# Kernel optimization log

Measured on AMD Instinct MI355X. Metric: run time of the kernel, lower is better.

Reference implementation:

```python
import jax, jax.numpy as jnp
import numpy as np

B, N, DIM, VDIM, H, HD = 4, 1369, 1024, 1536, 16, 64
ROPE_HW, ROPE_DIM, THETA = 37, 32, 10000.0
LN_EPS = 1e-5


def _rope_tables():
    # VisionRotaryEmbeddingFast: freqs_for='lang', dim=32, pt_seq_len=ft_seq_len=37
    inv = 1.0 / THETA ** (jnp.arange(0, ROPE_DIM, 2, dtype=jnp.float32) / ROPE_DIM)  # [16]
    t = jnp.arange(ROPE_HW, dtype=jnp.float32) / ROPE_HW * ROPE_HW                    # [37]
    f = t[:, None] * inv[None, :]                                                     # [37,16]
    f = jnp.repeat(f, 2, axis=-1)                                                     # [37,32]
    # broadcat along last dim over the 2D grid -> [37,37,64]
    f2 = jnp.concatenate([jnp.broadcast_to(f[:, None, :], (ROPE_HW, ROPE_HW, ROPE_DIM)),
                          jnp.broadcast_to(f[None, :, :], (ROPE_HW, ROPE_HW, ROPE_DIM))], axis=-1)
    f2 = f2.reshape(-1, 2 * ROPE_DIM)                                                 # [1369,64]
    return jnp.cos(f2), jnp.sin(f2)


def _rotate_half(x):
    # pairs (x0,x1) -> (-x1,x0), interleaved
    xr = x.reshape(*x.shape[:-1], x.shape[-1] // 2, 2)
    x1, x2 = xr[..., 0], xr[..., 1]
    return jnp.stack((-x2, x1), axis=-1).reshape(x.shape)


def setup_inputs() -> dict:
    key = jax.random.key(0)
    ks = jax.random.split(key, 8)
    return {
        "x": jax.random.normal(ks[0], (B, N, DIM), jnp.float32),
        "value": jax.random.normal(ks[1], (B, N, VDIM), jnp.float32),
        "attn_mask": jax.random.randint(ks[2], (B, N), 0, 2).astype(bool),
        "wq": jax.random.normal(ks[3], (DIM, DIM), jnp.float32) * 0.02,
        "wk": jax.random.normal(ks[4], (DIM, VDIM), jnp.float32) * 0.02,
        "wv": jax.random.normal(ks[5], (DIM, VDIM), jnp.float32) * 0.02,
        "ln_g": jnp.ones((DIM,), jnp.float32),
        "ln_b": jnp.zeros((DIM,), jnp.float32),
        "wp": jax.random.normal(ks[6], (DIM, DIM), jnp.float32) * 0.02,
        "bp": jnp.zeros((DIM,), jnp.float32),
    }


def reference(x, value, attn_mask, wq, wk, wv, ln_g, ln_b, wp, bp):
    cos, sin = _rope_tables()  # [N, 64] each
    # projections (torch F.linear: y = x @ W.T)
    q = jnp.einsum('bni,oi->bno', x, wq).reshape(B, N, H, HD).transpose(0, 2, 1, 3)
    k = jnp.einsum('bni,oi->bno', value, wk).reshape(B, N, H, HD).transpose(0, 2, 1, 3)
    v = jnp.einsum('bni,oi->bno', value, wv).reshape(B, N, H, HD).transpose(0, 2, 1, 3)
    # inline RoPE on q and k
    q = q * cos + _rotate_half(q) * sin
    k = k * cos + _rotate_half(k) * sin
    q = q * (HD ** -0.5)
    attn = jnp.einsum('bhnd,bhmd->bhnm', q, k)
    neg_inf = jnp.finfo(attn.dtype).min
    attn = jnp.where(attn_mask[:, None, None, :], attn, neg_inf)
    attn = jax.nn.softmax(attn, axis=-1)
    out = jnp.einsum('bhnm,bhmd->bhnd', attn, v)
    out = out.transpose(0, 2, 1, 3).reshape(B, N, H * HD)
    # inner_attn_ln (LayerNorm, eps=1e-5)
    mu = jnp.mean(out, axis=-1, keepdims=True)
    var = jnp.var(out, axis=-1, keepdims=True)
    out = (out - mu) * jax.lax.rsqrt(var + LN_EPS) * ln_g + ln_b
    # output projection
    return jnp.einsum('bni,oi->bno', out, wp) + bp
```

## Files before the change

kernel.cpp:

```cpp
#include <hip/hip_runtime.h>
#include <hip/hip_bf16.h>

#define BB 4
#define NN 1369
#define DIMM 1024
#define VDIMM 1536
#define HH 16
#define MM (BB*NN)
#define MPAD 5504
#define NPAD 1408
#define KVB 64
#define NT (NPAD/KVB)
#define QSCALE 0.18028334f

typedef __attribute__((ext_vector_type(4))) float f32x4;
typedef __attribute__((ext_vector_type(8))) __bf16 bf16x8;
typedef __attribute__((ext_vector_type(4))) __bf16 bf16x4;

#define GLOAD_LDS(gsrc, ldst) \
  __builtin_amdgcn_global_load_lds((const __attribute__((address_space(1))) unsigned int*)(gsrc), \
                                   (__attribute__((address_space(3))) unsigned int*)(ldst), 16, 0, 0)

__global__ __launch_bounds__(256) void cvt_inputs(const float* __restrict__ x,
                                                  const float* __restrict__ val,
                                                  __bf16* __restrict__ xb,
                                                  __bf16* __restrict__ vb) {
  const int NX = MM * 1024 / 4;
  const int NV = MM * 1536 / 4;
  int i = blockIdx.x * blockDim.x + threadIdx.x;
  int st = gridDim.x * blockDim.x;
  for (; i < NX + NV; i += st) {
    const float* s; __bf16* d; int j;
    if (i < NX) { s = x; d = xb; j = i; }
    else        { s = val; d = vb; j = i - NX; }
    f32x4 v = ((const f32x4*)s)[j];
    bf16x4 o;
    o[0] = (__bf16)v[0]; o[1] = (__bf16)v[1];
    o[2] = (__bf16)v[2]; o[3] = (__bf16)v[3];
    ((bf16x4*)d)[j] = o;
  }
}

__global__ __launch_bounds__(256) void cvt_weights(
    const float* __restrict__ wq, const float* __restrict__ wk,
    const float* __restrict__ wv, const float* __restrict__ wp,
    __bf16* __restrict__ wqb, __bf16* __restrict__ wkvb, __bf16* __restrict__ wpb) {
  const int NQ = 1024 * 1024 / 4;
  const int NK = 1024 * 1536 / 4;
  int i = blockIdx.x * blockDim.x + threadIdx.x;
  int st = gridDim.x * blockDim.x;
  for (; i < 2 * NQ + 2 * NK; i += st) {
    const float* s; __bf16* d; int j = i;
    if (j < NQ) { s = wq; d = wqb; }
    else if (j < NQ + NK) { j -= NQ; s = wk; d = wkvb; }
    else if (j < NQ + 2 * NK) { j -= NQ + NK; s = wv; d = wkvb + (size_t)1024 * 1536; }
    else { j -= NQ + 2 * NK; s = wp; d = wpb; }
    f32x4 v = ((const f32x4*)s)[j];
    bf16x4 o;
    o[0] = (__bf16)v[0]; o[1] = (__bf16)v[1];
    o[2] = (__bf16)v[2]; o[3] = (__bf16)v[3];
    ((bf16x4*)d)[j] = o;
  }
}

__global__ __launch_bounds__(256) void rope_tables(float* __restrict__ cosT,
                                                   float* __restrict__ sinT) {
  int idx = blockIdx.x * blockDim.x + threadIdx.x;
  if (idx >= NN * 64) return;
  int n = idx >> 6, d = idx & 63;
  int r = n / 37, c = n % 37;
  int m = (d < 32) ? (d >> 1) : ((d - 32) >> 1);
  float p = (d < 32) ? (float)r : (float)c;
  float inv = powf(10000.f, -(float)m * (1.f / 16.f));
  float a = p * inv;
  cosT[idx] = cosf(a);
  sinT[idx] = sinf(a);
}

__global__ __launch_bounds__(256) void mask_prep(const void* __restrict__ mask,
                                                 float* __restrict__ maskA) {
  __shared__ int flags[2];
  int t = threadIdx.x;
  if (t < 2) flags[t] = 0;
  __syncthreads();
  const unsigned int* mw = (const unsigned int*)mask;
  for (int i = t; i < NN; i += blockDim.x) {
    unsigned int w = mw[i];
    if (w == 0x3F800000u) atomicOr(&flags[1], 1);
    else if (w > 1u) atomicOr(&flags[0], 1);
  }
  __syncthreads();
  int md = flags[1] ? 2 : (flags[0] ? 1 : 0);
  const unsigned char* mb = (const unsigned char*)mask;
  const float* mf = (const float*)mask;
  for (int i = t; i < BB * NPAD; i += blockDim.x) {
    int b = i / NPAD, key = i % NPAD;
    float v = -1e30f;
    if (key < NN) {
      int idx = b * NN + key;
      bool on = (md == 0) ? (mw[idx] != 0u) : (md == 1) ? (mb[idx] != 0) : (mf[idx] != 0.f);
      if (on) v = 0.f;
    }
    maskA[i] = v;
  }
}

template <int TN, int EPI, int GRID2D>
__global__ __launch_bounds__(256) void gemm_bt(
    const __bf16* __restrict__ A, const __bf16* __restrict__ W, int K,
    __bf16* __restrict__ obf, __bf16* __restrict__ obf2, float* __restrict__ of32,
    const float* __restrict__ cosT, const float* __restrict__ sinT,
    const float* __restrict__ bp) {
  constexpr int MI = (TN == 128) ? 4 : 2;
  __shared__ __bf16 As[2][128 * 32];
  __shared__ __bf16 Bs[2][TN * 32];
  const int tid = threadIdx.x;
  const int w = tid >> 6, l = tid & 63;
  int tN, tM;
  if (GRID2D) {
    tN = blockIdx.x; tM = blockIdx.y;
  } else {
    const int i0 = blockIdx.x;
    const int orig = (i0 & 7) * 86 + (i0 >> 3);
    tN = orig & 15; tM = orig >> 4;
  }
  const int wm = (TN == 128) ? (w >> 1) : w;
  const int wn = (TN == 128) ? (w & 1) : 0;
  const int wmo = wm * ((TN == 128) ? 64 : 32);
  const int lo = l & 15, hi = l >> 4;

  const __bf16* Asrc = A + (size_t)(tM * 128 + lo) * K + hi * 8;
  const __bf16* Wsrc = W + (size_t)(tN * TN + lo) * K + hi * 8;

  f32x4 zero = {0.f, 0.f, 0.f, 0.f};
  f32x4 acc[MI][4];
#pragma unroll
  for (int i = 0; i < MI; ++i)
#pragma unroll
    for (int j = 0; j < 4; ++j) acc[i][j] = zero;

  auto GSTAGE = [&](int buf, int k0) {
#pragma unroll
    for (int j = 0; j < 2; ++j) {
      const int c = j * 4 + w;
      GLOAD_LDS(Asrc + (size_t)c * 16 * K + k0, (char*)&As[buf][c * 512]);
    }
    if constexpr (TN == 128) {
#pragma unroll
      for (int j = 0; j < 2; ++j) {
        const int c = j * 4 + w;
        GLOAD_LDS(Wsrc + (size_t)c * 16 * K + k0, (char*)&Bs[buf][c * 512]);
      }
    } else {
      GLOAD_LDS(Wsrc + (size_t)w * 16 * K + k0, (char*)&Bs[buf][w * 512]);
    }
  };

  const int nk = K >> 5;
  GSTAGE(0, 0);
  int cur = 0;
  const int ga = wmo >> 4;
  const int gb = (TN == 128) ? (wn * 4) : 0;
  for (int t = 0; t < nk; ++t) {
    __syncthreads();
    if (t + 1 < nk) GSTAGE(cur ^ 1, (t + 1) * 32);
    bf16x8 af[MI], bfr[4];
#pragma unroll
    for (int mi = 0; mi < MI; ++mi)
      af[mi] = *(const bf16x8*)&As[cur][(ga + mi) * 512 + hi * 128 + lo * 8];
#pragma unroll
    for (int ni = 0; ni < 4; ++ni)
      bfr[ni] = *(const bf16x8*)&Bs[cur][(gb + ni) * 512 + hi * 128 + lo * 8];
    __builtin_amdgcn_s_setprio(1);
#pragma unroll
    for (int mi = 0; mi < MI; ++mi)
#pragma unroll
      for (int ni = 0; ni < 4; ++ni)
        acc[mi][ni] = __builtin_amdgcn_mfma_f32_16x16x32_bf16(af[mi], bfr[ni], acc[mi][ni], 0, 0, 0);
    __builtin_amdgcn_s_setprio(0);
    cur ^= 1;
  }

  const int m_base = tM * 128 + wmo;
  const int o_base = tN * TN + wn * 64;
  const bool isK = (EPI == 1) && (tN < 8);
#pragma unroll
  for (int mi = 0; mi < MI; ++mi) {
    const int m4 = m_base + mi * 16 + hi * 4;
    if (EPI == 1 && !isK) {
      if (m4 < MM) {
        const int b0 = m4 / NN, n0 = m4 % NN;
#pragma unroll
        for (int ni = 0; ni < 4; ++ni) {
          const int o2 = o_base + ni * 16 + lo - 1024;
          const int h = o2 >> 6, d = o2 & 63;
          if (n0 <= NN - 4) {
            bf16x4 pv;
#pragma unroll
            for (int r = 0; r < 4; ++r) pv[r] = (__bf16)acc[mi][ni][r];
            *(bf16x4*)&obf2[((size_t)(b0 * HH + h) * 64 + d) * NPAD + n0] = pv;
          } else {
#pragma unroll
            for (int r = 0; r < 4; ++r) {
              const int mr = m4 + r;
              const int br = mr / NN, nr = mr % NN;
              obf2[((size_t)(br * HH + h) * 64 + d) * NPAD + nr] = (__bf16)acc[mi][ni][r];
            }
          }
        }
      }
    } else {
#pragma unroll
      for (int r = 0; r < 4; ++r) {
        const int mrow = m4 + r;
#pragma unroll
        for (int ni = 0; ni < 4; ++ni) {
          const int col = o_base + ni * 16 + lo;
          float v = acc[mi][ni][r];
          if (EPI == 0 || EPI == 1) {
            float pprt = __shfl_xor(v, 1);
            if (mrow < MM) {
              int b = mrow / NN, n = mrow % NN;
              int h = col >> 6, d = col & 63;
              float cs = cosT[n * 64 + d], sn = sinT[n * 64 + d];
              float out = v * cs + (((d & 1) == 0) ? -pprt : pprt) * sn;
              if (EPI == 0) out *= QSCALE;
              obf[((size_t)(b * HH + h) * NPAD + n) * 64 + d] = (__bf16)out;
            }
          } else {
            if (mrow < MM) of32[(size_t)mrow * DIMM + col] = v + bp[col];
          }
        }
      }
    }
  }
}

__device__ inline unsigned int pk2(float a, float b) {
  unsigned int ua = (unsigned int)__builtin_bit_cast(unsigned short, (__bf16)a);
  unsigned int ub = (unsigned int)__builtin_bit_cast(unsigned short, (__bf16)b);
  return ua | (ub << 16);
}

__global__ __launch_bounds__(256) void attn_kernel(
    const __bf16* __restrict__ Qb, const __bf16* __restrict__ Kb,
    const __bf16* __restrict__ Vtb, const float* __restrict__ maskA,
    float* __restrict__ AO) {
  __shared__ __bf16 Ks[2][64 * 64];
  __shared__ __bf16 Vs[2][64 * 64];
  __shared__ unsigned int Plds[4][16 * 32];
  const int tid = threadIdx.x;
  const int w = tid >> 6, l = tid & 63;
  const int lo = l & 15, hi = l >> 4;

  const int i = blockIdx.x;
  const int orig = (i & 7) * 176 + (i >> 3);
  const int bh = orig / NT;
  const int qt = orig % NT;
  const int b = bh >> 4;
  const int q0 = qt * 64 + w * 16;

  const __bf16* Qp = Qb + ((size_t)bh * NPAD + q0) * 64;
  bf16x8 qf0 = *(const bf16x8*)&Qp[lo * 64 + hi * 8];
  bf16x8 qf1 = *(const bf16x8*)&Qp[lo * 64 + 32 + hi * 8];

  const int row8 = l >> 3;
  const int swz16 = ((l & 7) ^ row8) << 4;
  const int lo7 = lo & 7;
  const int swzW = (lo & 7) << 2;

  f32x4 zero = {0.f, 0.f, 0.f, 0.f};
  f32x4 O[4];
#pragma unroll
  for (int n = 0; n < 4; ++n) O[n] = zero;
  float lr = 0.f;
  const float* mk = maskA + b * NPAD;

#define STAGE(buf, k0)                                                                   \
  {                                                                                      \
    _Pragma("unroll") for (int j = 0; j < 2; ++j) {                                      \
      const int rbase = (j * 4 + w) * 8;                                                 \
      const char* ksrc = (const char*)Kb +                                               \
          ((size_t)bh * NPAD + (k0) + rbase + row8) * 128 + swz16;                       \
      GLOAD_LDS(ksrc, (char*)&Ks[buf][0] + rbase * 128);                                 \
      const char* vsrc = (const char*)Vtb +                                              \
          ((size_t)(bh * 64 + rbase + row8) * NPAD + (k0)) * 2 + swz16;                  \
      GLOAD_LDS(vsrc, (char*)&Vs[buf][0] + rbase * 128);                                 \
    }                                                                                    \
  }

  STAGE(0, 0);
  __syncthreads();
  int cur = 0;

  for (int t = 0; t < NT; ++t) {
    if (t + 1 < NT) STAGE(cur ^ 1, (t + 1) * KVB);

    const __bf16* KB = &Ks[cur][0];
    const __bf16* VB = &Vs[cur][0];

    f32x4 mv[4];
#pragma unroll
    for (int c = 0; c < 4; ++c) mv[c] = *(const f32x4*)&mk[t * KVB + c * 16 + hi * 4];

    f32x4 S[4];
    __builtin_amdgcn_s_setprio(1);
#pragma unroll
    for (int c = 0; c < 4; ++c) {
      const int kr = c * 16 + lo;
      bf16x8 kfa = *(const bf16x8*)&KB[kr * 64 + ((hi ^ lo7) * 8)];
      bf16x8 kfb = *(const bf16x8*)&KB[kr * 64 + (((hi + 4) ^ lo7) * 8)];
      f32x4 s = __builtin_amdgcn_mfma_f32_16x16x32_bf16(kfa, qf0, zero, 0, 0, 0);
      S[c]     = __builtin_amdgcn_mfma_f32_16x16x32_bf16(kfb, qf1, s, 0, 0, 0);
    }
    __builtin_amdgcn_s_setprio(0);

    float rs = 0.f;
#pragma unroll
    for (int c = 0; c < 4; ++c) {
      float p0 = exp2f(S[c][0] + mv[c][0]);
      float p1 = exp2f(S[c][1] + mv[c][1]);
      float p2 = exp2f(S[c][2] + mv[c][2]);
      float p3 = exp2f(S[c][3] + mv[c][3]);
      rs += (p0 + p1) + (p2 + p3);
      uint2 pw = {pk2(p0, p1), pk2(p2, p3)};
      *(uint2*)&Plds[w][lo * 32 + ((8 * c + 2 * hi) ^ swzW)] = pw;
    }
    lr += rs;

    bf16x8 pf0 = *(const bf16x8*)&Plds[w][lo * 32 + ((4 * hi) ^ swzW)];
    bf16x8 pf1 = *(const bf16x8*)&Plds[w][lo * 32 + ((16 + 4 * hi) ^ swzW)];

    __builtin_amdgcn_s_setprio(1);
#pragma unroll
    for (int n = 0; n < 4; ++n) {
      const int vr = n * 16 + lo;
      bf16x8 vfa = *(const bf16x8*)&VB[vr * 64 + ((hi ^ lo7) * 8)];
      bf16x8 vfb = *(const bf16x8*)&VB[vr * 64 + (((hi + 4) ^ lo7) * 8)];
      O[n] = __builtin_amdgcn_mfma_f32_16x16x32_bf16(vfa, pf0, O[n], 0, 0, 0);
      O[n] = __builtin_amdgcn_mfma_f32_16x16x32_bf16(vfb, pf1, O[n], 0, 0, 0);
    }
    __builtin_amdgcn_s_setprio(0);

    __syncthreads();
    cur ^= 1;
  }
#undef STAGE

  lr += __shfl_xor(lr, 16);
  lr += __shfl_xor(lr, 32);
  const float inv = 1.f / lr;

  const int h = bh & 15;
  const int token = q0 + lo;
  if (token < NN) {
    float* dst = AO + (size_t)(b * NN + token) * DIMM + h * 64 + hi * 4;
#pragma unroll
    for (int n = 0; n < 4; ++n) {
      f32x4 o = O[n];
      o[0] *= inv; o[1] *= inv; o[2] *= inv; o[3] *= inv;
      *(f32x4*)(dst + n * 16) = o;
    }
  }
}

__global__ __launch_bounds__(256) void ln_kernel(
    const float* __restrict__ AO, const float* __restrict__ g,
    const float* __restrict__ be, __bf16* __restrict__ outb) {
  const int row = blockIdx.x;
  const int t = threadIdx.x;
  const float* x = AO + (size_t)row * DIMM;
  f32x4 v = ((const f32x4*)x)[t];
  float s = v[0] + v[1] + v[2] + v[3];
  float sq = v[0] * v[0] + v[1] * v[1] + v[2] * v[2] + v[3] * v[3];
#pragma unroll
  for (int m = 1; m < 64; m <<= 1) { s += __shfl_xor(s, m); sq += __shfl_xor(sq, m); }
  __shared__ float ss[4], ssq[4];
  int w = t >> 6, l = t & 63;
  if (l == 0) { ss[w] = s; ssq[w] = sq; }
  __syncthreads();
  s = ss[0] + ss[1] + ss[2] + ss[3];
  sq = ssq[0] + ssq[1] + ssq[2] + ssq[3];
  float mean = s * (1.f / 1024.f);
  float var = sq * (1.f / 1024.f) - mean * mean;
  float rstd = rsqrtf(var + 1e-5f);
  __bf16* o = outb + (size_t)row * DIMM + t * 4;
  const float* gp = g + t * 4;
  const float* bp2 = be + t * 4;
#pragma unroll
  for (int j = 0; j < 4; ++j) o[j] = (__bf16)((v[j] - mean) * rstd * gp[j] + bp2[j]);
}

extern "C" void kernel_launch(void* const* d_in, const int* in_sizes, int n_in,
                              void* d_out, int out_size, void* d_ws, size_t ws_size,
                              hipStream_t stream) {
  const float* x   = (const float*)d_in[0];
  const float* val = (const float*)d_in[1];
  const void*  msk = d_in[2];
  const float* wq  = (const float*)d_in[3];
  const float* wk  = (const float*)d_in[4];
  const float* wv  = (const float*)d_in[5];
  const float* lng = (const float*)d_in[6];
  const float* lnb = (const float*)d_in[7];
  const float* wp  = (const float*)d_in[8];
  const float* bpv = (const float*)d_in[9];
  float* out = (float*)d_out;

  char* ws = (char*)d_ws;
  size_t off = 0;
  auto alloc = [&](size_t bytes) -> char* {
    char* p = ws + off;
    off += (bytes + 255) & ~(size_t)255;
    return p;
  };
  __bf16* xb   = (__bf16*)alloc((size_t)MPAD * 1024 * 2);
  __bf16* vb   = (__bf16*)alloc((size_t)MPAD * 1536 * 2);
  __bf16* wqb  = (__bf16*)alloc((size_t)1024 * 1024 * 2);
  __bf16* wkvb = (__bf16*)alloc((size_t)2048 * 1536 * 2);
  __bf16* wpb  = (__bf16*)alloc((size_t)1024 * 1024 * 2);
  __bf16* Qb   = (__bf16*)alloc((size_t)64 * NPAD * 64 * 2);
  __bf16* Kb   = (__bf16*)alloc((size_t)64 * NPAD * 64 * 2);
  __bf16* Vtb  = (__bf16*)alloc((size_t)64 * 64 * NPAD * 2);
  float* AO    = (float*)alloc((size_t)MM * 1024 * 4);
  float* cosT  = (float*)alloc((size_t)NN * 64 * 4);
  float* sinT  = (float*)alloc((size_t)NN * 64 * 4);
  float* maskA = (float*)alloc((size_t)BB * NPAD * 4);


  cvt_inputs<<<2048, 256, 0, stream>>>(x, val, xb, vb);
  cvt_weights<<<1024, 256, 0, stream>>>(wq, wk, wv, wp, wqb, wkvb, wpb);
  rope_tables<<<(NN * 64 + 255) / 256, 256, 0, stream>>>(cosT, sinT);
  mask_prep<<<1, 256, 0, stream>>>(msk, maskA);

  gemm_bt<64, 0, 1><<<dim3(16, 43), 256, 0, stream>>>(xb, wqb, 1024, Qb, nullptr, nullptr, cosT, sinT, nullptr);
  gemm_bt<128, 1, 0><<<dim3(688), 256, 0, stream>>>(vb, wkvb, 1536, Kb, Vtb, nullptr, cosT, sinT, nullptr);

  attn_kernel<<<dim3(64 * NT), 256, 0, stream>>>(Qb, Kb, Vtb, maskA, AO);

  ln_kernel<<<MM, 256, 0, stream>>>(AO, lng, lnb, xb);

  gemm_bt<64, 3, 1><<<dim3(16, 43), 256, 0, stream>>>(xb, wpb, 1024, nullptr, nullptr, out, nullptr, nullptr, bpv);
}
```

Measured before the change: 281.5 us.

## Fold LayerNorm into output projection GEMM via precomputed row stats and column constants

```diff
diff --git a/kernel.cpp b/kernel.cpp
--- a/kernel.cpp
+++ b/kernel.cpp
@@ -44,64 +44,127 @@
 __global__ __launch_bounds__(256) void cvt_weights(
     const float* __restrict__ wq, const float* __restrict__ wk,
     const float* __restrict__ wv, const float* __restrict__ wp,
-    __bf16* __restrict__ wqb, __bf16* __restrict__ wkvb, __bf16* __restrict__ wpb) {
+    const float* __restrict__ g,
+    __bf16* __restrict__ wqb, __bf16* __restrict__ wkvb, __bf16* __restrict__ wgb) {
   const int NQ = 1024 * 1024 / 4;
   const int NK = 1024 * 1536 / 4;
   int i = blockIdx.x * blockDim.x + threadIdx.x;
   int st = gridDim.x * blockDim.x;
   for (; i < 2 * NQ + 2 * NK; i += st) {
-    const float* s; __bf16* d; int j = i;
-    if (j < NQ) { s = wq; d = wqb; }
-    else if (j < NQ + NK) { j -= NQ; s = wk; d = wkvb; }
-    else if (j < NQ + 2 * NK) { j -= NQ + NK; s = wv; d = wkvb + (size_t)1024 * 1536; }
-    else { j -= NQ + 2 * NK; s = wp; d = wpb; }
-    f32x4 v = ((const f32x4*)s)[j];
-    bf16x4 o;
-    o[0] = (__bf16)v[0]; o[1] = (__bf16)v[1];
-    o[2] = (__bf16)v[2]; o[3] = (__bf16)v[3];
-    ((bf16x4*)d)[j] = o;
-  }
-}
-
-__global__ __launch_bounds__(256) void rope_tables(float* __restrict__ cosT,
-                                                   float* __restrict__ sinT) {
-  int idx = blockIdx.x * blockDim.x + threadIdx.x;
-  if (idx >= NN * 64) return;
-  int n = idx >> 6, d = idx & 63;
-  int r = n / 37, c = n % 37;
-  int m = (d < 32) ? (d >> 1) : ((d - 32) >> 1);
-  float p = (d < 32) ? (float)r : (float)c;
-  float inv = powf(10000.f, -(float)m * (1.f / 16.f));
-  float a = p * inv;
-  cosT[idx] = cosf(a);
-  sinT[idx] = sinf(a);
-}
-
-__global__ __launch_bounds__(256) void mask_prep(const void* __restrict__ mask,
-                                                 float* __restrict__ maskA) {
-  __shared__ int flags[2];
-  int t = threadIdx.x;
-  if (t < 2) flags[t] = 0;
-  __syncthreads();
-  const unsigned int* mw = (const unsigned int*)mask;
-  for (int i = t; i < NN; i += blockDim.x) {
-    unsigned int w = mw[i];
-    if (w == 0x3F800000u) atomicOr(&flags[1], 1);
-    else if (w > 1u) atomicOr(&flags[0], 1);
-  }
-  __syncthreads();
-  int md = flags[1] ? 2 : (flags[0] ? 1 : 0);
-  const unsigned char* mb = (const unsigned char*)mask;
-  const float* mf = (const float*)mask;
-  for (int i = t; i < BB * NPAD; i += blockDim.x) {
-    int b = i / NPAD, key = i % NPAD;
-    float v = -1e30f;
-    if (key < NN) {
-      int idx = b * NN + key;
-      bool on = (md == 0) ? (mw[idx] != 0u) : (md == 1) ? (mb[idx] != 0) : (mf[idx] != 0.f);
-      if (on) v = 0.f;
-    }
-    maskA[i] = v;
+    int j = i;
+    if (j < NQ) {
+      f32x4 v = ((const f32x4*)wq)[j];
+      bf16x4 o;
+      o[0] = (__bf16)v[0]; o[1] = (__bf16)v[1]; o[2] = (__bf16)v[2]; o[3] = (__bf16)v[3];
+      ((bf16x4*)wqb)[j] = o;
+    } else if (j < NQ + NK) {
+      j -= NQ;
+      f32x4 v = ((const f32x4*)wk)[j];
+      bf16x4 o;
+      o[0] = (__bf16)v[0]; o[1] = (__bf16)v[1]; o[2] = (__bf16)v[2]; o[3] = (__bf16)v[3];
+      ((bf16x4*)wkvb)[j] = o;
+    } else if (j < NQ + 2 * NK) {
+      j -= NQ + NK;
+      f32x4 v = ((const f32x4*)wv)[j];
+      bf16x4 o;
+      o[0] = (__bf16)v[0]; o[1] = (__bf16)v[1]; o[2] = (__bf16)v[2]; o[3] = (__bf16)v[3];
+      ((bf16x4*)(wkvb + (size_t)1024 * 1536))[j] = o;
+    } else {
+      j -= NQ + 2 * NK;
+      f32x4 v = ((const f32x4*)wp)[j];
+      f32x4 gv = ((const f32x4*)g)[j & 255];
+      bf16x4 o;
+      o[0] = (__bf16)(v[0] * gv[0]); o[1] = (__bf16)(v[1] * gv[1]);
+      o[2] = (__bf16)(v[2] * gv[2]); o[3] = (__bf16)(v[3] * gv[3]);
+      ((bf16x4*)wgb)[j] = o;
+    }
+  }
+}
+
+__global__ __launch_bounds__(256) void c12_kernel(
+    const float* __restrict__ wp, const float* __restrict__ g,
+    const float* __restrict__ lnb, const float* __restrict__ bpv,
+    float* __restrict__ c1, float* __restrict__ c2) {
+  const int w = threadIdx.x >> 6, l = threadIdx.x & 63;
+  const int o = blockIdx.x * 4 + w;
+  const float* row = wp + (size_t)o * 1024;
+  float s1 = 0.f, s2 = 0.f;
+#pragma unroll
+  for (int j = 0; j < 4; ++j) {
+    const int idx = l * 4 + j * 256;
+    f32x4 wv = *(const f32x4*)&row[idx];
+    f32x4 gv = *(const f32x4*)&g[idx];
+    f32x4 bv = *(const f32x4*)&lnb[idx];
+#pragma unroll
+    for (int e = 0; e < 4; ++e) { s1 += wv[e] * gv[e]; s2 += wv[e] * bv[e]; }
+  }
+#pragma unroll
+  for (int m = 1; m < 64; m <<= 1) { s1 += __shfl_xor(s1, m); s2 += __shfl_xor(s2, m); }
+  if (l == 0) { c1[o] = s1; c2[o] = s2 + bpv[o]; }
+}
+
+__global__ __launch_bounds__(256) void stats_kernel(
+    const __bf16* __restrict__ AO, float* __restrict__ mu, float* __restrict__ rstd) {
+  const int w = threadIdx.x >> 6, l = threadIdx.x & 63;
+  const int row = blockIdx.x * 4 + w;
+  const __bf16* x = AO + (size_t)row * DIMM + l * 16;
+  float s = 0.f, sq = 0.f;
+#pragma unroll
+  for (int j = 0; j < 2; ++j) {
+    bf16x8 v = *(const bf16x8*)&x[j * 8];
+#pragma unroll
+    for (int e = 0; e < 8; ++e) { float f = (float)v[e]; s += f; sq += f * f; }
+  }
+#pragma unroll
+  for (int m = 1; m < 64; m <<= 1) { s += __shfl_xor(s, m); sq += __shfl_xor(sq, m); }
+  if (l == 0) {
+    float mean = s * (1.f / 1024.f);
+    mu[row] = mean;
+    rstd[row] = rsqrtf(sq * (1.f / 1024.f) - mean * mean + 1e-5f);
+  }
+}
+
+__global__ __launch_bounds__(256) void prep_aux(float* __restrict__ cosT,
+                                                float* __restrict__ sinT,
+                                                const void* __restrict__ mask,
+                                                float* __restrict__ maskA) {
+  const int blk = blockIdx.x;
+  if (blk < 343) {
+    int idx = blk * 256 + threadIdx.x;
+    if (idx >= NN * 64) return;
+    int n = idx >> 6, d = idx & 63;
+    int r = n / 37, c = n % 37;
+    int m = (d < 32) ? (d >> 1) : ((d - 32) >> 1);
+    float p = (d < 32) ? (float)r : (float)c;
+    float inv = powf(10000.f, -(float)m * (1.f / 16.f));
+    float a = p * inv;
+    cosT[idx] = cosf(a);
+    sinT[idx] = sinf(a);
+  } else {
+    __shared__ int flags[2];
+    int t = threadIdx.x;
+    if (t < 2) flags[t] = 0;
+    __syncthreads();
+    const unsigned int* mw = (const unsigned int*)mask;
+    for (int i = t; i < NN; i += blockDim.x) {
+      unsigned int w = mw[i];
+      if (w == 0x3F800000u) atomicOr(&flags[1], 1);
+      else if (w > 1u) atomicOr(&flags[0], 1);
+    }
+    __syncthreads();
+    int md = flags[1] ? 2 : (flags[0] ? 1 : 0);
+    const unsigned char* mb = (const unsigned char*)mask;
+    const float* mf = (const float*)mask;
+    for (int i = t; i < BB * NPAD; i += blockDim.x) {
+      int b = i / NPAD, key = i % NPAD;
+      float v = -1e30f;
+      if (key < NN) {
+        int idx = b * NN + key;
+        bool on = (md == 0) ? (mw[idx] != 0u) : (md == 1) ? (mb[idx] != 0) : (mf[idx] != 0.f);
+        if (on) v = 0.f;
+      }
+      maskA[i] = v;
+    }
   }
 }
 
@@ -110,7 +173,8 @@
     const __bf16* __restrict__ A, const __bf16* __restrict__ W, int K,
     __bf16* __restrict__ obf, __bf16* __restrict__ obf2, float* __restrict__ of32,
     const float* __restrict__ cosT, const float* __restrict__ sinT,
-    const float* __restrict__ bp) {
+    const float* __restrict__ mu, const float* __restrict__ rstd,
+    const float* __restrict__ c1, const float* __restrict__ c2) {
   constexpr int MI = (TN == 128) ? 4 : 2;
   __shared__ __bf16 As[2][128 * 32];
   __shared__ __bf16 Bs[2][TN * 32];
@@ -184,6 +248,14 @@
   const int m_base = tM * 128 + wmo;
   const int o_base = tN * TN + wn * 64;
   const bool isK = (EPI == 1) && (tN < 8);
+  float c1v[4], c2v[4];
+  if (EPI == 3) {
+#pragma unroll
+    for (int ni = 0; ni < 4; ++ni) {
+      c1v[ni] = c1[o_base + ni * 16 + lo];
+      c2v[ni] = c2[o_base + ni * 16 + lo];
+    }
+  }
 #pragma unroll
   for (int mi = 0; mi < MI; ++mi) {
     const int m4 = m_base + mi * 16 + hi * 4;
@@ -228,7 +300,9 @@
               obf[((size_t)(b * HH + h) * NPAD + n) * 64 + d] = (__bf16)out;
             }
           } else {
-            if (mrow < MM) of32[(size_t)mrow * DIMM + col] = v + bp[col];
+            if (mrow < MM)
+              of32[(size_t)mrow * DIMM + col] =
+                  rstd[mrow] * (v - mu[mrow] * c1v[ni]) + c2v[ni];
           }
         }
       }
@@ -245,7 +319,7 @@
 __global__ __launch_bounds__(256) void attn_kernel(
     const __bf16* __restrict__ Qb, const __bf16* __restrict__ Kb,
     const __bf16* __restrict__ Vtb, const float* __restrict__ maskA,
-    float* __restrict__ AO) {
+    __bf16* __restrict__ AO) {
   __shared__ __bf16 Ks[2][64 * 64];
   __shared__ __bf16 Vs[2][64 * 64];
   __shared__ unsigned int Plds[4][16 * 32];
@@ -354,41 +428,15 @@
   const int h = bh & 15;
   const int token = q0 + lo;
   if (token < NN) {
-    float* dst = AO + (size_t)(b * NN + token) * DIMM + h * 64 + hi * 4;
+    __bf16* dst = AO + (size_t)(b * NN + token) * DIMM + h * 64 + hi * 4;
 #pragma unroll
     for (int n = 0; n < 4; ++n) {
-      f32x4 o = O[n];
-      o[0] *= inv; o[1] *= inv; o[2] *= inv; o[3] *= inv;
-      *(f32x4*)(dst + n * 16) = o;
-    }
-  }
-}
-
-__global__ __launch_bounds__(256) void ln_kernel(
-    const float* __restrict__ AO, const float* __restrict__ g,
-    const float* __restrict__ be, __bf16* __restrict__ outb) {
-  const int row = blockIdx.x;
-  const int t = threadIdx.x;
-  const float* x = AO + (size_t)row * DIMM;
-  f32x4 v = ((const f32x4*)x)[t];
-  float s = v[0] + v[1] + v[2] + v[3];
-  float sq = v[0] * v[0] + v[1] * v[1] + v[2] * v[2] + v[3] * v[3];
-#pragma unroll
-  for (int m = 1; m < 64; m <<= 1) { s += __shfl_xor(s, m); sq += __shfl_xor(sq, m); }
-  __shared__ float ss[4], ssq[4];
-  int w = t >> 6, l = t & 63;
-  if (l == 0) { ss[w] = s; ssq[w] = sq; }
-  __syncthreads();
-  s = ss[0] + ss[1] + ss[2] + ss[3];
-  sq = ssq[0] + ssq[1] + ssq[2] + ssq[3];
-  float mean = s * (1.f / 1024.f);
-  float var = sq * (1.f / 1024.f) - mean * mean;
-  float rstd = rsqrtf(var + 1e-5f);
-  __bf16* o = outb + (size_t)row * DIMM + t * 4;
-  const float* gp = g + t * 4;
-  const float* bp2 = be + t * 4;
-#pragma unroll
-  for (int j = 0; j < 4; ++j) o[j] = (__bf16)((v[j] - mean) * rstd * gp[j] + bp2[j]);
+      bf16x4 o;
+#pragma unroll
+      for (int e = 0; e < 4; ++e) o[e] = (__bf16)(O[n][e] * inv);
+      *(bf16x4*)(dst + n * 16) = o;
+    }
+  }
 }
 
 extern "C" void kernel_launch(void* const* d_in, const int* in_sizes, int n_in,
@@ -417,27 +465,34 @@
   __bf16* vb   = (__bf16*)alloc((size_t)MPAD * 1536 * 2);
   __bf16* wqb  = (__bf16*)alloc((size_t)1024 * 1024 * 2);
   __bf16* wkvb = (__bf16*)alloc((size_t)2048 * 1536 * 2);
-  __bf16* wpb  = (__bf16*)alloc((size_t)1024 * 1024 * 2);
+  __bf16* wgb  = (__bf16*)alloc((size_t)1024 * 1024 * 2);
   __bf16* Qb   = (__bf16*)alloc((size_t)64 * NPAD * 64 * 2);
   __bf16* Kb   = (__bf16*)alloc((size_t)64 * NPAD * 64 * 2);
   __bf16* Vtb  = (__bf16*)alloc((size_t)64 * 64 * NPAD * 2);
-  float* AO    = (float*)alloc((size_t)MM * 1024 * 4);
+  __bf16* AO   = (__bf16*)alloc((size_t)MPAD * 1024 * 2);
   float* cosT  = (float*)alloc((size_t)NN * 64 * 4);
   float* sinT  = (float*)alloc((size_t)NN * 64 * 4);
   float* maskA = (float*)alloc((size_t)BB * NPAD * 4);
+  float* muv   = (float*)alloc((size_t)MM * 4);
+  float* rstdv = (float*)alloc((size_t)MM * 4);
+  float* c1v   = (float*)alloc((size_t)1024 * 4);
+  float* c2v   = (float*)alloc((size_t)1024 * 4);
 
 
   cvt_inputs<<<2048, 256, 0, stream>>>(x, val, xb, vb);
-  cvt_weights<<<1024, 256, 0, stream>>>(wq, wk, wv, wp, wqb, wkvb, wpb);
-  rope_tables<<<(NN * 64 + 255) / 256, 256, 0, stream>>>(cosT, sinT);
-  mask_prep<<<1, 256, 0, stream>>>(msk, maskA);
-
-  gemm_bt<64, 0, 1><<<dim3(16, 43), 256, 0, stream>>>(xb, wqb, 1024, Qb, nullptr, nullptr, cosT, sinT, nullptr);
-  gemm_bt<128, 1, 0><<<dim3(688), 256, 0, stream>>>(vb, wkvb, 1536, Kb, Vtb, nullptr, cosT, sinT, nullptr);
+  cvt_weights<<<1024, 256, 0, stream>>>(wq, wk, wv, wp, lng, wqb, wkvb, wgb);
+  prep_aux<<<344, 256, 0, stream>>>(cosT, sinT, msk, maskA);
+  c12_kernel<<<256, 256, 0, stream>>>(wp, lng, lnb, bpv, c1v, c2v);
+
+  gemm_bt<64, 0, 1><<<dim3(16, 43), 256, 0, stream>>>(xb, wqb, 1024, Qb, nullptr, nullptr,
+                                                      cosT, sinT, nullptr, nullptr, nullptr, nullptr);
+  gemm_bt<128, 1, 0><<<dim3(688), 256, 0, stream>>>(vb, wkvb, 1536, Kb, Vtb, nullptr,
+                                                    cosT, sinT, nullptr, nullptr, nullptr, nullptr);
 
   attn_kernel<<<dim3(64 * NT), 256, 0, stream>>>(Qb, Kb, Vtb, maskA, AO);
 
-  ln_kernel<<<MM, 256, 0, stream>>>(AO, lng, lnb, xb);
-
-  gemm_bt<64, 3, 1><<<dim3(16, 43), 256, 0, stream>>>(xb, wpb, 1024, nullptr, nullptr, out, nullptr, nullptr, bpv);
-}
+  stats_kernel<<<MM / 4, 256, 0, stream>>>(AO, muv, rstdv);
+
+  gemm_bt<64, 3, 1><<<dim3(16, 43), 256, 0, stream>>>(AO, wgb, 1024, nullptr, nullptr, out,
+                                                      nullptr, nullptr, muv, rstdv, c1v, c2v);
+}
```

Result: no change. 277.1 us (-1.6%).
